# Kernel tuning notes

Measured on AMD Instinct MI355X. Metric: run time of the kernel, lower is better.

## Reference

```python
import jax, jax.numpy as jnp
import numpy as np

N, E, K, F, R = 100000, 200000, 16, 32, 2
EPS = 1e-5

def setup_inputs() -> dict:
    key = jax.random.key(0)
    ks = jax.random.split(key, 32)
    inp = {}
    inp['x'] = jax.random.normal(ks[0], (N, F), jnp.float32)
    inp['y'] = jax.random.normal(ks[1], (E, F), jnp.float32)
    inp['deg_g'] = jax.random.uniform(ks[2], (N, 1), jnp.float32)
    inp['deg_lg'] = jax.random.uniform(ks[3], (E, 1), jnp.float32)
    inp['t_g'] = jax.random.randint(ks[4], (N, K), 0, N)
    inp['tt_g'] = jax.random.randint(ks[5], (N, K), 0, N)
    inp['t_lg'] = jax.random.randint(ks[6], (E, K), 0, E)
    inp['tt_lg'] = jax.random.randint(ks[7], (E, K), 0, E)
    inp['dst'] = jax.random.randint(ks[8], (E,), 0, N)
    inp['pm_pd'] = jax.random.randint(ks[9], (E,), 0, N)
    i = [10]
    def mk(shape):
        a = jax.random.normal(ks[i[0]], shape, jnp.float32) * 0.1
        i[0] += 1
        return a
    for nm in ['theta_x', 'theta_deg', 'theta_y', 'gamma_y', 'gamma_deg', 'gamma_x']:
        inp[nm + '_w'] = mk((F, F)); inp[nm + '_b'] = mk((F,))
    inp['theta_r_w'] = mk((R, F, F)); inp['theta_r_b'] = mk((R, F))
    inp['gamma_r_w'] = mk((R, F, F)); inp['gamma_r_b'] = mk((R, F))
    inp['bn_x_w'] = jnp.ones((F,), jnp.float32); inp['bn_x_b'] = jnp.zeros((F,), jnp.float32)
    inp['bn_y_w'] = jnp.ones((F,), jnp.float32); inp['bn_y_b'] = jnp.zeros((F,), jnp.float32)
    return inp

def _lin(a, w, b):
    return a @ w + b

def _bn(a, w, b):
    # BatchNorm1d in training mode: biased batch stats
    m = a.mean(axis=0)
    v = a.var(axis=0)
    return (a - m) / jnp.sqrt(v + EPS) * w + b

def _aggregate(z, t, tt):
    # per-node gather+sum over neighbor index lists (t: radius-0, tt: radius-1)
    return jnp.stack([z[t].sum(axis=1), z[tt].sum(axis=1)])  # [R, M, F]

def reference(x, y, deg_g, deg_lg, t_g, tt_g, t_lg, tt_lg, dst, pm_pd,
              theta_x_w, theta_x_b, theta_deg_w, theta_deg_b, theta_y_w, theta_y_b,
              gamma_y_w, gamma_y_b, gamma_deg_w, gamma_deg_b, gamma_x_w, gamma_x_b,
              theta_r_w, theta_r_b, gamma_r_w, gamma_r_b,
              bn_x_w, bn_x_b, bn_y_w, bn_y_b):
    n = F // 2
    pmpd_x = x[pm_pd]                                   # [E, F] embedding gather
    zs = _aggregate(x, t_g, tt_g)                        # [R, N, F]
    sum_x = jnp.einsum('rnf,rfo->no', zs, theta_r_w) + theta_r_b.sum(axis=0)
    pmpd_y = jax.ops.segment_sum(y, dst, num_segments=x.shape[0])  # copy_edge + sum
    xo = (_lin(x, theta_x_w, theta_x_b)
          + _lin(deg_g * x, theta_deg_w, theta_deg_b)
          + sum_x
          + _lin(pmpd_y, theta_y_w, theta_y_b))
    xo = jnp.concatenate([xo[:, :n], jax.nn.relu(xo[:, n:])], axis=1)
    xo = _bn(xo, bn_x_w, bn_x_b)
    zy = _aggregate(y, t_lg, tt_lg)                      # [R, E, F]
    sum_y = jnp.einsum('ref,rfo->eo', zy, gamma_r_w) + gamma_r_b.sum(axis=0)
    yo = (_lin(y, gamma_y_w, gamma_y_b)
          + _lin(deg_lg * y, gamma_deg_w, gamma_deg_b)
          + sum_y
          + _lin(pmpd_x, gamma_x_w, gamma_x_b))
    yo = jnp.concatenate([yo[:, :n], jax.nn.relu(yo[:, n:])], axis=1)
    yo = _bn(yo, bn_y_w, bn_y_b)
    return xo, yo
```

## Files before the change

kernel.cpp:

```cpp
#include <hip/hip_runtime.h>

#define NN 100000
#define NE 200000
#define MT (NN + NE)

typedef unsigned short u16;
typedef __attribute__((ext_vector_type(8))) short bf16x8;
typedef __attribute__((ext_vector_type(4))) float f32x4;

__device__ __forceinline__ float bf2f(u16 u) {
    union { unsigned int i; float f; } v; v.i = ((unsigned int)u) << 16; return v.f;
}
__device__ __forceinline__ u16 f2bf(float f) {
    union { unsigned int i; float f; } v; v.f = f;
    unsigned int r = v.i + 0x7fffu + ((v.i >> 16) & 1u);
    return (u16)(r >> 16);
}
__device__ __forceinline__ void unpack2(unsigned int u, float& lo, float& hi) {
    union { unsigned int i; float f; } a, b;
    a.i = u << 16; b.i = u & 0xffff0000u;
    lo = a.f; hi = b.f;
}
__device__ __forceinline__ unsigned int pack2(float a, float b) {
    return (unsigned int)f2bf(a) | ((unsigned int)f2bf(b) << 16);
}
__device__ __forceinline__ float loadf(const void* p, size_t i, int f32) {
    return f32 ? ((const float*)p)[i] : bf2f(((const u16*)p)[i]);
}
__device__ __forceinline__ void acc8(float a[8], uint4 g) {
    float e0, e1, e2, e3, e4, e5, e6, e7;
    unpack2(g.x, e0, e1); unpack2(g.y, e2, e3);
    unpack2(g.z, e4, e5); unpack2(g.w, e6, e7);
    a[0] += e0; a[1] += e1; a[2] += e2; a[3] += e3;
    a[4] += e4; a[5] += e5; a[6] += e6; a[7] += e7;
}

__global__ void detect_kernel(const unsigned int* __restrict__ x, int* flag) {
    __shared__ int cnt;
    if (threadIdx.x == 0) cnt = 0;
    __syncthreads();
    int bad = 0;
    for (int i = threadIdx.x; i < 1024; i += 256) {
        unsigned int e = (x[i] >> 7) & 0xFF;
        if (e == 0xFF || (e > 0 && (e < 107 || e > 134))) bad++;
    }
    atomicAdd(&cnt, bad);
    __syncthreads();
    if (threadIdx.x == 0) *flag = (cnt > 256) ? 1 : 0;
}

__global__ __launch_bounds__(256) void prep_kernel(
    const void* txw, const void* tdw, const void* tyw,
    const void* gyw, const void* gdw, const void* gxw,
    const void* trw, const void* grw,
    const void* txb, const void* tdb, const void* tyb,
    const void* gyb, const void* gdb, const void* gxb,
    const void* trb, const void* grb,
    u16* Bfx, u16* Bfy, float* bx, float* by, const int* flagp)
{
    int f32 = *flagp;
    int t = blockIdx.x * 256 + threadIdx.x;
    if (t < 4096) {
        int b = t >> 9, lane = (t >> 3) & 63, j = t & 7;
        int m = b >> 1;
        int k = ((lane >> 4) << 3) + j;
        int f = ((b & 1) << 4) + (lane & 15);
        size_t idx = (size_t)k * 32 + f;
        float v = (m == 0) ? loadf(txw, idx, f32) : (m == 1) ? loadf(tdw, idx, f32)
                : (m == 2) ? loadf(trw, idx, f32) : loadf(trw, 1024 + idx, f32);
        Bfx[t] = f2bf(v);
    } else if (t < 10240) {
        int e = t - 4096;
        int b = e >> 9, lane = (e >> 3) & 63, j = e & 7;
        int m = b >> 1;
        int k = ((lane >> 4) << 3) + j;
        int f = ((b & 1) << 4) + (lane & 15);
        size_t idx = (size_t)k * 32 + f;
        float v = (m == 0) ? loadf(gyw, idx, f32) : (m == 1) ? loadf(gdw, idx, f32)
                : (m == 2) ? loadf(grw, idx, f32) : (m == 3) ? loadf(grw, 1024 + idx, f32)
                : (m == 4) ? loadf(gxw, idx, f32) : loadf(tyw, idx, f32);
        Bfy[e] = f2bf(v);
    } else if (t < 10304) {
        int f = t - 10240;
        if (f < 32) {
            bx[f] = loadf(txb, f, f32) + loadf(tdb, f, f32) + loadf(tyb, f, f32)
                  + loadf(trb, f, f32) + loadf(trb, 32 + f, f32);
        } else {
            f -= 32;
            by[f] = loadf(gyb, f, f32) + loadf(gdb, f, f32) + loadf(gxb, f, f32)
                  + loadf(grb, f, f32) + loadf(grb, 32 + f, f32);
        }
    }
}

__global__ __launch_bounds__(256) void convert_kernel(
    const void* __restrict__ x, const void* __restrict__ y,
    u16* __restrict__ xb, u16* __restrict__ yb, const int* __restrict__ flagp)
{
    int f32 = *flagp;
    int t = blockIdx.x * 256 + threadIdx.x;
    if (t < NN * 4) {
        int r = t >> 2, q = t & 3;
        uint4 o;
        if (f32) {
            const float4* fp = (const float4*)((const float*)x + (size_t)r * 32 + q * 8);
            float4 v0 = fp[0], v1 = fp[1];
            o.x = pack2(v0.x, v0.y); o.y = pack2(v0.z, v0.w);
            o.z = pack2(v1.x, v1.y); o.w = pack2(v1.z, v1.w);
        } else {
            o = *(const uint4*)((const u16*)x + (size_t)r * 32 + q * 8);
        }
        *(uint4*)(xb + (size_t)r * 32 + q * 8) = o;
    } else if (t < MT * 4) {
        int t2 = t - NN * 4;
        int r = t2 >> 2, q = t2 & 3;
        uint4 o;
        if (f32) {
            const float4* fp = (const float4*)((const float*)y + (size_t)r * 32 + q * 8);
            float4 v0 = fp[0], v1 = fp[1];
            o.x = pack2(v0.x, v0.y); o.y = pack2(v0.z, v0.w);
            o.z = pack2(v1.x, v1.y); o.w = pack2(v1.z, v1.w);
        } else {
            o = *(const uint4*)((const u16*)y + (size_t)r * 32 + q * 8);
        }
        *(uint4*)(yb + (size_t)r * 32 + q * 8) = o;
    }
}

template<int IS_Y>
__device__ __forceinline__ void fused_body(
    const u16* __restrict__ xb, const u16* __restrict__ yb,
    float* xacc,
    const u16* __restrict__ Bf, const float* __restrict__ bias,
    const void* __restrict__ deg,
    const int* __restrict__ tl, const int* __restrict__ ttl,
    const int* __restrict__ pm_pd, const int* __restrict__ dst,
    float* __restrict__ xmfma, u16* __restrict__ ypre,
    float* __restrict__ ystats, int f32, int sb,
    int* s_t, int* s_tt, float* s_sum, float* s_sq)
{
    const int M = IS_Y ? NE : NN;
    int row0 = sb * 64;
    if (row0 >= M) return;
    if (IS_Y && threadIdx.x < 32) { s_sum[threadIdx.x] = 0.f; s_sq[threadIdx.x] = 0.f; }
    int lim = (M - row0) * 16;
    for (int i = threadIdx.x; i < 1024; i += 256) {
        int v  = (i < lim) ? __builtin_nontemporal_load(&tl[(size_t)row0 * 16 + i])  : 0;
        int v2 = (i < lim) ? __builtin_nontemporal_load(&ttl[(size_t)row0 * 16 + i]) : 0;
        int si = (i >> 4) * 17 + (i & 15);
        s_t[si] = v; s_tt[si] = v2;
    }
    __syncthreads();
    int lane = threadIdx.x & 63, wib = threadIdx.x >> 6;
    int r0 = row0 + wib * 16;
    if (r0 + 16 <= M) {
        const u16* tab = IS_Y ? yb : xb;
        int m = lane & 15, q = lane >> 4;
        int gr = r0 + m;
        const int* il  = &s_t[(wib * 16 + m) * 17];
        const int* ill = &s_tt[(wib * 16 + m) * 17];

        bf16x8 selfv = *(const bf16x8*)(tab + (size_t)gr * 32 + q * 8);
        union { u16 s[8]; bf16x8 v; } pm;
        if (IS_Y) {
            int ai = pm_pd[gr];
            pm.v = *(const bf16x8*)(xb + (size_t)ai * 32 + q * 8);
        }

        float aT[8]  = {0.f, 0.f, 0.f, 0.f, 0.f, 0.f, 0.f, 0.f};
        float aTT[8] = {0.f, 0.f, 0.f, 0.f, 0.f, 0.f, 0.f, 0.f};
        uint4 ga[8], gb[8];
#pragma unroll
        for (int j = 0; j < 8; ++j)
            ga[j] = *(const uint4*)(tab + (size_t)il[j] * 32 + q * 8);
#pragma unroll
        for (int j = 0; j < 8; ++j)
            gb[j] = *(const uint4*)(tab + (size_t)il[8 + j] * 32 + q * 8);
#pragma unroll
        for (int j = 0; j < 8; ++j) acc8(aT, ga[j]);
#pragma unroll
        for (int j = 0; j < 8; ++j)
            ga[j] = *(const uint4*)(tab + (size_t)ill[j] * 32 + q * 8);
#pragma unroll
        for (int j = 0; j < 8; ++j) acc8(aT, gb[j]);
#pragma unroll
        for (int j = 0; j < 8; ++j)
            gb[j] = *(const uint4*)(tab + (size_t)ill[8 + j] * 32 + q * 8);
#pragma unroll
        for (int j = 0; j < 8; ++j) acc8(aTT, ga[j]);
#pragma unroll
        for (int j = 0; j < 8; ++j) acc8(aTT, gb[j]);

        union { u16 s[8]; bf16x8 v; } ft, ftt;
#pragma unroll
        for (int j = 0; j < 8; ++j) { ft.s[j] = f2bf(aT[j]); ftt.s[j] = f2bf(aTT[j]); }

        const u16* bp = Bf + lane * 8;
#define BFR(b) (*(const bf16x8*)(bp + (b) * 512))
        f32x4 z = {0.f, 0.f, 0.f, 0.f};
        f32x4 a0, a1, d0, d1, c0 = z, c1 = z;
        a0 = __builtin_amdgcn_mfma_f32_16x16x32_bf16(selfv, BFR(0), z, 0, 0, 0);
        a1 = __builtin_amdgcn_mfma_f32_16x16x32_bf16(selfv, BFR(1), z, 0, 0, 0);
        d0 = __builtin_amdgcn_mfma_f32_16x16x32_bf16(selfv, BFR(2), z, 0, 0, 0);
        d1 = __builtin_amdgcn_mfma_f32_16x16x32_bf16(selfv, BFR(3), z, 0, 0, 0);
        a0 = __builtin_amdgcn_mfma_f32_16x16x32_bf16(ft.v,  BFR(4), a0, 0, 0, 0);
        a1 = __builtin_amdgcn_mfma_f32_16x16x32_bf16(ft.v,  BFR(5), a1, 0, 0, 0);
        a0 = __builtin_amdgcn_mfma_f32_16x16x32_bf16(ftt.v, BFR(6), a0, 0, 0, 0);
        a1 = __builtin_amdgcn_mfma_f32_16x16x32_bf16(ftt.v, BFR(7), a1, 0, 0, 0);
        if (IS_Y) {
            a0 = __builtin_amdgcn_mfma_f32_16x16x32_bf16(pm.v,  BFR(8),  a0, 0, 0, 0);
            a1 = __builtin_amdgcn_mfma_f32_16x16x32_bf16(pm.v,  BFR(9),  a1, 0, 0, 0);
            c0 = __builtin_amdgcn_mfma_f32_16x16x32_bf16(selfv, BFR(10), z, 0, 0, 0);
            c1 = __builtin_amdgcn_mfma_f32_16x16x32_bf16(selfv, BFR(11), z, 0, 0, 0);
        }
#undef BFR

        int n = m;
        int rowb = r0 + q * 4;
        float bl_ = bias[n], bh_ = bias[16 + n];
        float s0 = 0.f, q0 = 0.f, s1 = 0.f, q1 = 0.f;
#pragma unroll
        for (int i = 0; i < 4; ++i) {
            float dgi = loadf(deg, rowb + i, f32);
            size_t ro = (size_t)(rowb + i) * 32;
            float lo = a0[i] + dgi * d0[i] + bl_;
            float hi = a1[i] + dgi * d1[i] + bh_;
            if (!IS_Y) {
                __builtin_nontemporal_store(lo, &xmfma[ro + n]);
                __builtin_nontemporal_store(hi, &xmfma[ro + 16 + n]);
            } else {
                hi = fmaxf(hi, 0.f);
                __builtin_nontemporal_store(f2bf(lo), &ypre[ro + n]);
                __builtin_nontemporal_store(f2bf(hi), &ypre[ro + 16 + n]);
                int d = dst[rowb + i];
                float* p = xacc + (size_t)d * 32;
                atomicAdd(p + n,      c0[i]);
                atomicAdd(p + 16 + n, c1[i]);
                s0 += lo; q0 += lo * lo;
                s1 += hi; q1 += hi * hi;
            }
        }
        if (IS_Y) {
            s0 += __shfl_xor(s0, 16); s0 += __shfl_xor(s0, 32);
            q0 += __shfl_xor(q0, 16); q0 += __shfl_xor(q0, 32);
            s1 += __shfl_xor(s1, 16); s1 += __shfl_xor(s1, 32);
            q1 += __shfl_xor(q1, 16); q1 += __shfl_xor(q1, 32);
            if (lane < 16) {
                atomicAdd(&s_sum[n], s0);      atomicAdd(&s_sq[n], q0);
                atomicAdd(&s_sum[16 + n], s1); atomicAdd(&s_sq[16 + n], q1);
            }
        }
    }
    if (IS_Y) {
        __syncthreads();
        if (threadIdx.x < 32) {
            atomicAdd(&ystats[threadIdx.x], s_sum[threadIdx.x]);
            atomicAdd(&ystats[32 + threadIdx.x], s_sq[threadIdx.x]);
        }
    }
}

__global__ __launch_bounds__(256, 3) void fused_both(
    const u16* __restrict__ xb, const u16* __restrict__ yb, float* xacc,
    const u16* __restrict__ Bfx, const u16* __restrict__ Bfy,
    const float* __restrict__ bx, const float* __restrict__ by,
    const void* __restrict__ deg_g, const void* __restrict__ deg_lg,
    const int* __restrict__ t_g, const int* __restrict__ tt_g,
    const int* __restrict__ t_lg, const int* __restrict__ tt_lg,
    const int* __restrict__ pm_pd, const int* __restrict__ dst,
    float* __restrict__ xmfma, u16* __restrict__ ypre,
    float* __restrict__ stats, const int* __restrict__ flagp)
{
    __shared__ int s_t[1088];
    __shared__ int s_tt[1088];
    __shared__ float s_sum[32];
    __shared__ float s_sq[32];
    int f32 = *flagp;
    int bid = blockIdx.x;
    int s = bid % 3;
    if (s == 2) {
        fused_body<0>(xb, yb, xacc, Bfx, bx, deg_g, t_g, tt_g, pm_pd, dst,
                      xmfma, ypre, stats, f32, bid / 3,
                      s_t, s_tt, s_sum, s_sq);
    } else {
        fused_body<1>(xb, yb, xacc, Bfy, by, deg_lg, t_lg, tt_lg, pm_pd, dst,
                      xmfma, ypre, stats + 64, f32, (bid / 3) * 2 + s,
                      s_t, s_tt, s_sum, s_sq);
    }
}

__global__ __launch_bounds__(256) void xstats_kernel(
    const float* __restrict__ xmfma, const float* __restrict__ xacc,
    float* __restrict__ stats)
{
    __shared__ float s_sum[32];
    __shared__ float s_sq[32];
    if (threadIdx.x < 32) { s_sum[threadIdx.x] = 0.f; s_sq[threadIdx.x] = 0.f; }
    __syncthreads();
    int tid = blockIdx.x * 256 + threadIdx.x;
    int fq = (tid & 7) * 4;
    float4 a = ((const float4*)xmfma)[tid];
    float4 b = ((const float4*)xacc)[tid];
    float sv[4], qv[4];
    sv[0] = a.x + b.x; sv[1] = a.y + b.y; sv[2] = a.z + b.z; sv[3] = a.w + b.w;
    if (fq >= 16) {
#pragma unroll
        for (int i = 0; i < 4; ++i) sv[i] = fmaxf(sv[i], 0.f);
    }
#pragma unroll
    for (int i = 0; i < 4; ++i) qv[i] = sv[i] * sv[i];
#pragma unroll
    for (int off = 8; off < 64; off <<= 1) {
#pragma unroll
        for (int i = 0; i < 4; ++i) {
            sv[i] += __shfl_xor(sv[i], off);
            qv[i] += __shfl_xor(qv[i], off);
        }
    }
    int lane = threadIdx.x & 63;
    if (lane < 8) {
        int f0 = lane * 4;
#pragma unroll
        for (int i = 0; i < 4; ++i) {
            atomicAdd(&s_sum[f0 + i], sv[i]);
            atomicAdd(&s_sq[f0 + i], qv[i]);
        }
    }
    __syncthreads();
    if (threadIdx.x < 32) {
        atomicAdd(&stats[threadIdx.x], s_sum[threadIdx.x]);
        atomicAdd(&stats[32 + threadIdx.x], s_sq[threadIdx.x]);
    }
}

__global__ void finalize_stats(
    const float* stats,
    const void* bnxw, const void* bnxb, const void* bnyw, const void* bnyb,
    float* scsh, const int* flagp)
{
    int f32 = *flagp;
    int f = threadIdx.x;
    if (f < 32) {
        float m = stats[f] / (float)NN;
        float var = stats[32 + f] / (float)NN - m * m;
        float inv = rsqrtf(var + 1e-5f);
        float sc = loadf(bnxw, f, f32) * inv;
        scsh[f] = sc; scsh[32 + f] = loadf(bnxb, f, f32) - m * sc;
    } else if (f < 64) {
        int g = f - 32;
        float m = stats[64 + g] / (float)NE;
        float var = stats[96 + g] / (float)NE - m * m;
        float inv = rsqrtf(var + 1e-5f);
        float sc = loadf(bnyw, g, f32) * inv;
        scsh[64 + g] = sc; scsh[96 + g] = loadf(bnyb, g, f32) - m * sc;
    }
}

__global__ __launch_bounds__(256) void apply_bn(
    const float* __restrict__ xmfma, const float* __restrict__ xacc,
    const u16* __restrict__ ypre,
    const float* __restrict__ scsh, void* __restrict__ out,
    const int* __restrict__ flagp)
{
    int f32 = *flagp;
    int tid = blockIdx.x * 256 + threadIdx.x;
    if (tid >= MT * 8) return;
    int fq = (tid & 7) * 4;
    const float* sc;
    float4 v;
    if (tid < NN * 8) {
        float4 a = ((const float4*)xmfma)[tid];
        float4 b = ((const float4*)xacc)[tid];
        v.x = a.x + b.x; v.y = a.y + b.y; v.z = a.z + b.z; v.w = a.w + b.w;
        if (fq >= 16) {
            v.x = fmaxf(v.x, 0.f); v.y = fmaxf(v.y, 0.f);
            v.z = fmaxf(v.z, 0.f); v.w = fmaxf(v.w, 0.f);
        }
        sc = scsh;
    } else {
        size_t off = (size_t)tid * 4 - (size_t)NN * 32;
        ushort4 u = *(const ushort4*)(ypre + off);
        v.x = bf2f(u.x); v.y = bf2f(u.y); v.z = bf2f(u.z); v.w = bf2f(u.w);
        sc = scsh + 64;
    }
    float o0 = v.x * sc[fq + 0] + sc[32 + fq + 0];
    float o1 = v.y * sc[fq + 1] + sc[32 + fq + 1];
    float o2 = v.z * sc[fq + 2] + sc[32 + fq + 2];
    float o3 = v.w * sc[fq + 3] + sc[32 + fq + 3];
    if (f32) {
        float4 o; o.x = o0; o.y = o1; o.z = o2; o.w = o3;
        ((float4*)out)[tid] = o;
    } else {
        ushort4 o; o.x = f2bf(o0); o.y = f2bf(o1); o.z = f2bf(o2); o.w = f2bf(o3);
        ((ushort4*)out)[tid] = o;
    }
}

extern "C" void kernel_launch(void* const* d_in, const int* in_sizes, int n_in,
                              void* d_out, int out_size, void* d_ws, size_t ws_size,
                              hipStream_t stream)
{
    const void* x      = d_in[0];
    const void* y      = d_in[1];
    const void* deg_g  = d_in[2];
    const void* deg_lg = d_in[3];
    const int* t_g   = (const int*)d_in[4];
    const int* tt_g  = (const int*)d_in[5];
    const int* t_lg  = (const int*)d_in[6];
    const int* tt_lg = (const int*)d_in[7];
    const int* dst   = (const int*)d_in[8];
    const int* pm_pd = (const int*)d_in[9];

    char* ws = (char*)d_ws;
    int*   flag = (int*)ws;
    u16* Bfx   = (u16*)(ws + 256);
    u16* Bfy   = Bfx + 4096;
    float* bx  = (float*)(ws + 24576);
    float* by  = bx + 32;
    float* stats = by + 32;
    float* scsh  = stats + 128;
    u16* xb    = (u16*)(ws + 65536);
    u16* yb    = xb + (size_t)NN * 32;
    float* xacc = (float*)(yb + (size_t)NE * 32);
    u16* ypre  = (u16*)(xacc + (size_t)NN * 32);
    float* xmfma = (float*)(ypre + (size_t)NE * 32);

    hipMemsetAsync(stats, 0, 256 * sizeof(float), stream);
    hipMemsetAsync(xacc, 0, (size_t)NN * 32 * sizeof(float), stream);

    detect_kernel<<<1, 256, 0, stream>>>((const unsigned int*)x, flag);
    prep_kernel<<<41, 256, 0, stream>>>(
        d_in[10], d_in[12], d_in[14], d_in[16], d_in[18], d_in[20],
        d_in[22], d_in[24],
        d_in[11], d_in[13], d_in[15], d_in[17], d_in[19], d_in[21],
        d_in[23], d_in[25],
        Bfx, Bfy, bx, by, flag);
    convert_kernel<<<4688, 256, 0, stream>>>(x, y, xb, yb, flag);
    fused_both<<<4689, 256, 0, stream>>>(xb, yb, xacc, Bfx, Bfy, bx, by,
                                         deg_g, deg_lg, t_g, tt_g, t_lg, tt_lg,
                                         pm_pd, dst, xmfma, ypre, stats, flag);
    xstats_kernel<<<3125, 256, 0, stream>>>(xmfma, xacc, stats);
    finalize_stats<<<1, 64, 0, stream>>>(stats, d_in[26], d_in[27], d_in[28],
                                         d_in[29], scsh, flag);
    apply_bn<<<9375, 256, 0, stream>>>(xmfma, xacc, ypre, scsh, d_out, flag);
}
```

Before: 437.2 us.

## Merge setup kernels, drop xmfma buffer via atomics, fold stats finalize into apply

Detection, weight prep, input conversion and workspace zeroing now run in one prep_convert kernel, replacing two memsets and three launches. Every block re-runs the format detection locally. The x-side MFMA result is atomically added into xacc instead of going to a separate xmfma buffer, which removes a 12.8MB write and two reads of it. The BN scale/shift finalize is computed per block inside apply_bn, removing another launch. In exchange there are 6.4M extra float atomics on xacc, which contend with the scatter atomics already there, plus redundant detect and finalize work in each block.

```diff
diff --git a/kernel.cpp b/kernel.cpp
--- a/kernel.cpp
+++ b/kernel.cpp
@@ -35,72 +35,42 @@
     a[4] += e4; a[5] += e5; a[6] += e6; a[7] += e7;
 }
 
-__global__ void detect_kernel(const unsigned int* __restrict__ x, int* flag) {
-    __shared__ int cnt;
-    if (threadIdx.x == 0) cnt = 0;
+__device__ __forceinline__ int detect_local(const unsigned int* x, int* s_cnt) {
+    if (threadIdx.x == 0) *s_cnt = 0;
     __syncthreads();
     int bad = 0;
     for (int i = threadIdx.x; i < 1024; i += 256) {
         unsigned int e = (x[i] >> 7) & 0xFF;
         if (e == 0xFF || (e > 0 && (e < 107 || e > 134))) bad++;
     }
-    atomicAdd(&cnt, bad);
-    __syncthreads();
-    if (threadIdx.x == 0) *flag = (cnt > 256) ? 1 : 0;
-}
-
-__global__ __launch_bounds__(256) void prep_kernel(
+    atomicAdd(s_cnt, bad);
+    __syncthreads();
+    return (*s_cnt > 256) ? 1 : 0;
+}
+
+__global__ __launch_bounds__(256) void prep_convert(
+    const void* __restrict__ x, const void* __restrict__ y,
     const void* txw, const void* tdw, const void* tyw,
     const void* gyw, const void* gdw, const void* gxw,
     const void* trw, const void* grw,
     const void* txb, const void* tdb, const void* tyb,
     const void* gyb, const void* gdb, const void* gxb,
     const void* trb, const void* grb,
-    u16* Bfx, u16* Bfy, float* bx, float* by, const int* flagp)
-{
-    int f32 = *flagp;
-    int t = blockIdx.x * 256 + threadIdx.x;
-    if (t < 4096) {
-        int b = t >> 9, lane = (t >> 3) & 63, j = t & 7;
-        int m = b >> 1;
-        int k = ((lane >> 4) << 3) + j;
-        int f = ((b & 1) << 4) + (lane & 15);
-        size_t idx = (size_t)k * 32 + f;
-        float v = (m == 0) ? loadf(txw, idx, f32) : (m == 1) ? loadf(tdw, idx, f32)
-                : (m == 2) ? loadf(trw, idx, f32) : loadf(trw, 1024 + idx, f32);
-        Bfx[t] = f2bf(v);
-    } else if (t < 10240) {
-        int e = t - 4096;
-        int b = e >> 9, lane = (e >> 3) & 63, j = e & 7;
-        int m = b >> 1;
-        int k = ((lane >> 4) << 3) + j;
-        int f = ((b & 1) << 4) + (lane & 15);
-        size_t idx = (size_t)k * 32 + f;
-        float v = (m == 0) ? loadf(gyw, idx, f32) : (m == 1) ? loadf(gdw, idx, f32)
-                : (m == 2) ? loadf(grw, idx, f32) : (m == 3) ? loadf(grw, 1024 + idx, f32)
-                : (m == 4) ? loadf(gxw, idx, f32) : loadf(tyw, idx, f32);
-        Bfy[e] = f2bf(v);
-    } else if (t < 10304) {
-        int f = t - 10240;
-        if (f < 32) {
-            bx[f] = loadf(txb, f, f32) + loadf(tdb, f, f32) + loadf(tyb, f, f32)
-                  + loadf(trb, f, f32) + loadf(trb, 32 + f, f32);
-        } else {
-            f -= 32;
-            by[f] = loadf(gyb, f, f32) + loadf(gdb, f, f32) + loadf(gxb, f, f32)
-                  + loadf(grb, f, f32) + loadf(grb, 32 + f, f32);
-        }
-    }
-}
-
-__global__ __launch_bounds__(256) void convert_kernel(
-    const void* __restrict__ x, const void* __restrict__ y,
-    u16* __restrict__ xb, u16* __restrict__ yb, const int* __restrict__ flagp)
-{
-    int f32 = *flagp;
-    int t = blockIdx.x * 256 + threadIdx.x;
-    if (t < NN * 4) {
-        int r = t >> 2, q = t & 3;
+    u16* __restrict__ xb, u16* __restrict__ yb, float* __restrict__ xacc,
+    u16* Bfx, u16* Bfy, float* bx, float* by,
+    float* __restrict__ stats, int* flagp)
+{
+    __shared__ int s_cnt;
+    int f32 = detect_local((const unsigned int*)x, &s_cnt);
+    size_t t = (size_t)blockIdx.x * 256 + threadIdx.x;
+    if (t == 0) *flagp = f32;
+    if (t < 256) stats[t] = 0.f;
+    if (t < 800000) {
+        float4 z4; z4.x = 0.f; z4.y = 0.f; z4.z = 0.f; z4.w = 0.f;
+        ((float4*)xacc)[t] = z4;
+    }
+    if (t < (size_t)NN * 4) {
+        int r = (int)(t >> 2), q = (int)(t & 3);
         uint4 o;
         if (f32) {
             const float4* fp = (const float4*)((const float*)x + (size_t)r * 32 + q * 8);
@@ -111,9 +81,9 @@
             o = *(const uint4*)((const u16*)x + (size_t)r * 32 + q * 8);
         }
         *(uint4*)(xb + (size_t)r * 32 + q * 8) = o;
-    } else if (t < MT * 4) {
-        int t2 = t - NN * 4;
-        int r = t2 >> 2, q = t2 & 3;
+    } else if (t < (size_t)MT * 4) {
+        size_t t2 = t - (size_t)NN * 4;
+        int r = (int)(t2 >> 2), q = (int)(t2 & 3);
         uint4 o;
         if (f32) {
             const float4* fp = (const float4*)((const float*)y + (size_t)r * 32 + q * 8);
@@ -124,6 +94,39 @@
             o = *(const uint4*)((const u16*)y + (size_t)r * 32 + q * 8);
         }
         *(uint4*)(yb + (size_t)r * 32 + q * 8) = o;
+    } else if (t < (size_t)MT * 4 + 10304) {
+        int e = (int)(t - (size_t)MT * 4);
+        if (e < 4096) {
+            int b = e >> 9, lane = (e >> 3) & 63, j = e & 7;
+            int m = b >> 1;
+            int k = ((lane >> 4) << 3) + j;
+            int f = ((b & 1) << 4) + (lane & 15);
+            size_t idx = (size_t)k * 32 + f;
+            float v = (m == 0) ? loadf(txw, idx, f32) : (m == 1) ? loadf(tdw, idx, f32)
+                    : (m == 2) ? loadf(trw, idx, f32) : loadf(trw, 1024 + idx, f32);
+            Bfx[e] = f2bf(v);
+        } else if (e < 10240) {
+            int e2 = e - 4096;
+            int b = e2 >> 9, lane = (e2 >> 3) & 63, j = e2 & 7;
+            int m = b >> 1;
+            int k = ((lane >> 4) << 3) + j;
+            int f = ((b & 1) << 4) + (lane & 15);
+            size_t idx = (size_t)k * 32 + f;
+            float v = (m == 0) ? loadf(gyw, idx, f32) : (m == 1) ? loadf(gdw, idx, f32)
+                    : (m == 2) ? loadf(grw, idx, f32) : (m == 3) ? loadf(grw, 1024 + idx, f32)
+                    : (m == 4) ? loadf(gxw, idx, f32) : loadf(tyw, idx, f32);
+            Bfy[e2] = f2bf(v);
+        } else {
+            int f = e - 10240;
+            if (f < 32) {
+                bx[f] = loadf(txb, f, f32) + loadf(tdb, f, f32) + loadf(tyb, f, f32)
+                      + loadf(trb, f, f32) + loadf(trb, 32 + f, f32);
+            } else {
+                f -= 32;
+                by[f] = loadf(gyb, f, f32) + loadf(gdb, f, f32) + loadf(gxb, f, f32)
+                      + loadf(grb, f, f32) + loadf(grb, 32 + f, f32);
+            }
+        }
     }
 }
 
@@ -135,7 +138,7 @@
     const void* __restrict__ deg,
     const int* __restrict__ tl, const int* __restrict__ ttl,
     const int* __restrict__ pm_pd, const int* __restrict__ dst,
-    float* __restrict__ xmfma, u16* __restrict__ ypre,
+    u16* __restrict__ ypre,
     float* __restrict__ ystats, int f32, int sb,
     int* s_t, int* s_tt, float* s_sum, float* s_sq)
 {
@@ -226,8 +229,8 @@
             float lo = a0[i] + dgi * d0[i] + bl_;
             float hi = a1[i] + dgi * d1[i] + bh_;
             if (!IS_Y) {
-                __builtin_nontemporal_store(lo, &xmfma[ro + n]);
-                __builtin_nontemporal_store(hi, &xmfma[ro + 16 + n]);
+                atomicAdd(&xacc[ro + n],      lo);
+                atomicAdd(&xacc[ro + 16 + n], hi);
             } else {
                 hi = fmaxf(hi, 0.f);
                 __builtin_nontemporal_store(f2bf(lo), &ypre[ro + n]);
@@ -268,7 +271,7 @@
     const int* __restrict__ t_g, const int* __restrict__ tt_g,
     const int* __restrict__ t_lg, const int* __restrict__ tt_lg,
     const int* __restrict__ pm_pd, const int* __restrict__ dst,
-    float* __restrict__ xmfma, u16* __restrict__ ypre,
+    u16* __restrict__ ypre,
     float* __restrict__ stats, const int* __restrict__ flagp)
 {
     __shared__ int s_t[1088];
@@ -280,18 +283,17 @@
     int s = bid % 3;
     if (s == 2) {
         fused_body<0>(xb, yb, xacc, Bfx, bx, deg_g, t_g, tt_g, pm_pd, dst,
-                      xmfma, ypre, stats, f32, bid / 3,
+                      ypre, stats, f32, bid / 3,
                       s_t, s_tt, s_sum, s_sq);
     } else {
         fused_body<1>(xb, yb, xacc, Bfy, by, deg_lg, t_lg, tt_lg, pm_pd, dst,
-                      xmfma, ypre, stats + 64, f32, (bid / 3) * 2 + s,
+                      ypre, stats + 64, f32, (bid / 3) * 2 + s,
                       s_t, s_tt, s_sum, s_sq);
     }
 }
 
 __global__ __launch_bounds__(256) void xstats_kernel(
-    const float* __restrict__ xmfma, const float* __restrict__ xacc,
-    float* __restrict__ stats)
+    const float* __restrict__ xacc, float* __restrict__ stats)
 {
     __shared__ float s_sum[32];
     __shared__ float s_sq[32];
@@ -299,10 +301,9 @@
     __syncthreads();
     int tid = blockIdx.x * 256 + threadIdx.x;
     int fq = (tid & 7) * 4;
-    float4 a = ((const float4*)xmfma)[tid];
     float4 b = ((const float4*)xacc)[tid];
     float sv[4], qv[4];
-    sv[0] = a.x + b.x; sv[1] = a.y + b.y; sv[2] = a.z + b.z; sv[3] = a.w + b.w;
+    sv[0] = b.x; sv[1] = b.y; sv[2] = b.z; sv[3] = b.w;
     if (fq >= 16) {
 #pragma unroll
         for (int i = 0; i < 4; ++i) sv[i] = fmaxf(sv[i], 0.f);
@@ -333,55 +334,50 @@
     }
 }
 
-__global__ void finalize_stats(
-    const float* stats,
-    const void* bnxw, const void* bnxb, const void* bnyw, const void* bnyb,
-    float* scsh, const int* flagp)
-{
+__global__ __launch_bounds__(256) void apply_bn(
+    const float* __restrict__ xacc, const u16* __restrict__ ypre,
+    const float* __restrict__ stats,
+    const void* __restrict__ bnxw, const void* __restrict__ bnxb,
+    const void* __restrict__ bnyw, const void* __restrict__ bnyb,
+    void* __restrict__ out, const int* __restrict__ flagp)
+{
+    __shared__ float s_sc[128];
     int f32 = *flagp;
-    int f = threadIdx.x;
-    if (f < 32) {
-        float m = stats[f] / (float)NN;
-        float var = stats[32 + f] / (float)NN - m * m;
-        float inv = rsqrtf(var + 1e-5f);
-        float sc = loadf(bnxw, f, f32) * inv;
-        scsh[f] = sc; scsh[32 + f] = loadf(bnxb, f, f32) - m * sc;
-    } else if (f < 64) {
-        int g = f - 32;
-        float m = stats[64 + g] / (float)NE;
-        float var = stats[96 + g] / (float)NE - m * m;
-        float inv = rsqrtf(var + 1e-5f);
-        float sc = loadf(bnyw, g, f32) * inv;
-        scsh[64 + g] = sc; scsh[96 + g] = loadf(bnyb, g, f32) - m * sc;
-    }
-}
-
-__global__ __launch_bounds__(256) void apply_bn(
-    const float* __restrict__ xmfma, const float* __restrict__ xacc,
-    const u16* __restrict__ ypre,
-    const float* __restrict__ scsh, void* __restrict__ out,
-    const int* __restrict__ flagp)
-{
-    int f32 = *flagp;
+    if (threadIdx.x < 64) {
+        int f = threadIdx.x;
+        if (f < 32) {
+            float m = stats[f] / (float)NN;
+            float var = stats[32 + f] / (float)NN - m * m;
+            float inv = rsqrtf(var + 1e-5f);
+            float sc = loadf(bnxw, f, f32) * inv;
+            s_sc[f] = sc; s_sc[32 + f] = loadf(bnxb, f, f32) - m * sc;
+        } else {
+            int g = f - 32;
+            float m = stats[64 + g] / (float)NE;
+            float var = stats[96 + g] / (float)NE - m * m;
+            float inv = rsqrtf(var + 1e-5f);
+            float sc = loadf(bnyw, g, f32) * inv;
+            s_sc[64 + g] = sc; s_sc[96 + g] = loadf(bnyb, g, f32) - m * sc;
+        }
+    }
+    __syncthreads();
     int tid = blockIdx.x * 256 + threadIdx.x;
     if (tid >= MT * 8) return;
     int fq = (tid & 7) * 4;
     const float* sc;
     float4 v;
     if (tid < NN * 8) {
-        float4 a = ((const float4*)xmfma)[tid];
-        float4 b = ((const float4*)xacc)[tid];
-        v.x = a.x + b.x; v.y = a.y + b.y; v.z = a.z + b.z; v.w = a.w + b.w;
+        v = ((const float4*)xacc)[tid];
         if (fq >= 16) {
             v.x = fmaxf(v.x, 0.f); v.y = fmaxf(v.y, 0.f);
             v.z = fmaxf(v.z, 0.f); v.w = fmaxf(v.w, 0.f);
         }
-        sc = scsh;
+        sc = s_sc;
     } else {
         size_t off = (size_t)tid * 4 - (size_t)NN * 32;
         ushort4 u = *(const ushort4*)(ypre + off);
         v.x = bf2f(u.x); v.y = bf2f(u.y); v.z = bf2f(u.z); v.w = bf2f(u.w);
-        sc = scsh + 64;
+        sc = s_sc + 64;
     }
     float o0 = v.x * sc[fq + 0] + sc[32 + fq + 0];
     float o1 = v.y * sc[fq + 1] + sc[32 + fq + 1];
@@ -418,29 +414,23 @@
     float* bx  = (float*)(ws + 24576);
     float* by  = bx + 32;
     float* stats = by + 32;
-    float* scsh  = stats + 128;
     u16* xb    = (u16*)(ws + 65536);
     u16* yb    = xb + (size_t)NN * 32;
     float* xacc = (float*)(yb + (size_t)NE * 32);
     u16* ypre  = (u16*)(xacc + (size_t)NN * 32);
-    float* xmfma = (float*)(ypre + (size_t)NE * 32);
-
-    hipMemsetAsync(stats, 0, 256 * sizeof(float), stream);
-    hipMemsetAsync(xacc, 0, (size_t)NN * 32 * sizeof(float), stream);
-
-    detect_kernel<<<1, 256, 0, stream>>>((const unsigned int*)x, flag);
-    prep_kernel<<<41, 256, 0, stream>>>(
+
+    prep_convert<<<4728, 256, 0, stream>>>(
+        x, y,
         d_in[10], d_in[12], d_in[14], d_in[16], d_in[18], d_in[20],
         d_in[22], d_in[24],
         d_in[11], d_in[13], d_in[15], d_in[17], d_in[19], d_in[21],
         d_in[23], d_in[25],
-        Bfx, Bfy, bx, by, flag);
-    convert_kernel<<<4688, 256, 0, stream>>>(x, y, xb, yb, flag);
+        xb, yb, xacc, Bfx, Bfy, bx, by, stats, flag);
     fused_both<<<4689, 256, 0, stream>>>(xb, yb, xacc, Bfx, Bfy, bx, by,
                                          deg_g, deg_lg, t_g, tt_g, t_lg, tt_lg,
-                                         pm_pd, dst, xmfma, ypre, stats, flag);
-    xstats_kernel<<<3125, 256, 0, stream>>>(xmfma, xacc, stats);
-    finalize_stats<<<1, 64, 0, stream>>>(stats, d_in[26], d_in[27], d_in[28],
-                                         d_in[29], scsh, flag);
-    apply_bn<<<9375, 256, 0, stream>>>(xmfma, xacc, ypre, scsh, d_out, flag);
-}
+                                         pm_pd, dst, ypre, stats, flag);
+    xstats_kernel<<<3125, 256, 0, stream>>>(xacc, stats);
+    apply_bn<<<9375, 256, 0, stream>>>(xacc, ypre, stats,
+                                       d_in[26], d_in[27], d_in[28], d_in[29],
+                                       d_out, flag);
+}
```

Result: no change. 431.4 us (-1.3%).
